# Kernel optimization log

Measured on AMD Instinct MI355X. Metric: run time of the kernel, lower is better.

The kernel has to match this reference:

```python
import jax, jax.numpy as jnp
import numpy as np

HID = 2048
HEADS = 16
HD = HID // HEADS  # 128
EPS = 1e-6


def setup_inputs() -> dict:
    key = jax.random.key(0)
    ks = jax.random.split(key, 9)
    s = 1.0 / np.sqrt(HID)
    return {
        "hidden_states": jax.random.normal(ks[0], (4, 4096, HID), jnp.float32),
        "q_w": jax.random.normal(ks[1], (HID, HID), jnp.float32) * s,
        "q_b": jnp.zeros((HID,), jnp.float32),
        "k_w": jax.random.normal(ks[2], (HID, HID), jnp.float32) * s,
        "k_b": jnp.zeros((HID,), jnp.float32),
        "v_w": jax.random.normal(ks[3], (HID, HID), jnp.float32) * s,
        "v_b": jnp.zeros((HID,), jnp.float32),
        "o_w": jax.random.normal(ks[4], (HID, HID), jnp.float32) * s,
        "o_b": jnp.zeros((HID,), jnp.float32),
    }


def _heads(x, b, s):
    # [B,S,HID] -> [B,H,S,Dh]
    return x.reshape(b, s, HEADS, HD).transpose(0, 2, 1, 3)


def reference(hidden_states, q_w, q_b, k_w, k_b, v_w, v_b, o_w, o_b):
    b, s, _ = hidden_states.shape
    # torch Linear: y = x @ W.T + b
    q = _heads(hidden_states @ q_w.T + q_b, b, s)
    k = _heads(hidden_states @ k_w.T + k_b, b, s)
    v = _heads(hidden_states @ v_w.T + v_b, b, s)
    # kernel feature map: elu(x) + 1
    qp = jax.nn.elu(q) + 1.0
    kp = jax.nn.elu(k) + 1.0
    # KV outer-product reduction over sequence: [B,H,Dh,Dh]
    kv = jnp.einsum('bhsd,bhse->bhde', kp, v)
    # normalizer z = q' @ sum_s k'  -> [B,H,S,1]
    z = jnp.einsum('bhsd,bhd->bhs', qp, kp.sum(axis=2))[..., None]
    attn = jnp.einsum('bhsd,bhde->bhse', qp, kv) / (z + EPS)
    out = attn.transpose(0, 2, 1, 3).reshape(b, s, HID)
    return out @ o_w.T + o_b
```

## Files before the change

### kernel.cpp

```cpp
#include <hip/hip_runtime.h>
#include <hip/hip_bf16.h>

#define HIDC 2048
#define NHEADS 16
#define HDIM 128
#define NB 4
#define NS 4096
#define NROWS (NB*NS)
#define QSTR 6144
#define EPSV 1e-6f

typedef __attribute__((ext_vector_type(8))) short s16x8;
typedef __attribute__((ext_vector_type(4))) float f32x4;
typedef __attribute__((ext_vector_type(8))) unsigned short u16x8;

static __device__ __forceinline__ unsigned short f2b(float f) {
  unsigned int u = __float_as_uint(f);
  u += 0x7fffu + ((u >> 16) & 1u);
  return (unsigned short)(u >> 16);
}
static __device__ __forceinline__ float b2f(unsigned short h) {
  return __uint_as_float(((unsigned int)h) << 16);
}

static __device__ __forceinline__ void gload_lds16(const unsigned short* g, unsigned short* l) {
  __builtin_amdgcn_global_load_lds(
      (const __attribute__((address_space(1))) void*)g,
      (__attribute__((address_space(3))) void*)l, 16, 0, 0);
}

__global__ __launch_bounds__(256) void convert_all(
    const float* __restrict__ hs, const float* __restrict__ qw,
    const float* __restrict__ kw, const float* __restrict__ vw,
    const float* __restrict__ ow,
    unsigned short* __restrict__ hsb, unsigned short* __restrict__ qwb,
    unsigned short* __restrict__ kwb, unsigned short* __restrict__ vwb,
    unsigned short* __restrict__ owb)
{
  int bid = blockIdx.x;
  const float* src; unsigned short* dst; size_t base;
  if (bid < 16384) { src = hs; dst = hsb; base = (size_t)bid << 11; }
  else {
    int t = bid - 16384; int wsel = t >> 11; int wb = t & 2047;
    src = wsel == 0 ? qw : wsel == 1 ? kw : wsel == 2 ? vw : ow;
    dst = wsel == 0 ? qwb : wsel == 1 ? kwb : wsel == 2 ? vwb : owb;
    base = (size_t)wb << 11;
  }
  size_t i = base + ((size_t)threadIdx.x << 3);
  float4 a = *(const float4*)(src + i);
  float4 b = *(const float4*)(src + i + 4);
  u16x8 o;
  o[0] = f2b(a.x); o[1] = f2b(a.y); o[2] = f2b(a.z); o[3] = f2b(a.w);
  o[4] = f2b(b.x); o[5] = f2b(b.y); o[6] = f2b(b.z); o[7] = f2b(b.w);
  *(u16x8*)(dst + i) = o;
}

template<int QKV, int OUT_BF16>
__global__ __launch_bounds__(512, 2) void gemm256(
    const unsigned short* __restrict__ A,
    const unsigned short* __restrict__ B0,
    const unsigned short* __restrict__ B1,
    const unsigned short* __restrict__ B2,
    const float* __restrict__ bias0,
    const float* __restrict__ bias1,
    const float* __restrict__ bias2,
    void* __restrict__ Cp,
    int ntile, int astr, int ostr)
{
  __shared__ unsigned short lds[65536];
  const int tid = threadIdx.x;
  const int lane = tid & 63, wid = tid >> 6;
  const int wr = wid >> 2, wc = wid & 3;
  const int l15 = lane & 15, l4 = lane >> 4;

  const int cpx = (int)gridDim.x >> 3;
  const int bidx = (int)blockIdx.x;
  const int wg = (bidx & 7) * cpx + (bidx >> 3);
  const int csz = ntile << 2;
  const int chunk = wg / csz;
  const int t = wg % csz;
  const int bm = ((chunk << 2) + (t & 3)) << 8;
  const int bn = (t >> 2) << 8;

  const unsigned short* Bp = B0;
  const float* bias = bias0;
  bool act = false;
  int bnw = bn;
  if (QKV) {
    int seg = bn >> 11;
    Bp = seg == 0 ? B0 : (seg == 1 ? B1 : B2);
    bias = seg == 0 ? bias0 : (seg == 1 ? bias1 : bias2);
    act = seg < 2;
    bnw = bn & 2047;
  }

  const int c0 = wid << 1;
  const int srow = lane >> 2;
  const int scol = (((lane & 3) ^ ((srow >> 1) & 3)) << 3);
  const unsigned short* Asrc0 = A + (size_t)(bm + (c0 << 4) + srow) * astr + scol;
  const unsigned short* Asrc1 = Asrc0 + (size_t)16 * astr;
  const unsigned short* Bsrc0 = Bp + (size_t)(bnw + (c0 << 4) + srow) * HIDC + scol;
  const unsigned short* Bsrc1 = Bsrc0 + (size_t)16 * HIDC;
  const int adst = c0 << 9;

  const int xa = ((l4 ^ ((l15 >> 1) & 3)) << 3);
  const int abase = ((wr << 7) + l15) * 32 + xa;
  const int bbase = 8192 + ((wc << 6) + l15) * 32 + xa;

  f32x4 acc[8][4] = {};
  s16x8 bfr[2][4];
  s16x8 alo[2][4];
  s16x8 ahi[4];

#define STAGE_A(s_) { const int sl_ = ((s_) & 3) << 14; const int kt_ = (s_) << 5; \
    gload_lds16(Asrc0 + kt_, &lds[sl_ + adst]); \
    gload_lds16(Asrc1 + kt_, &lds[sl_ + adst + 512]); }
#define STAGE_B(s_) { const int sl_ = ((s_) & 3) << 14; const int kt_ = (s_) << 5; \
    gload_lds16(Bsrc0 + kt_, &lds[sl_ + 8192 + adst]); \
    gload_lds16(Bsrc1 + kt_, &lds[sl_ + 8192 + adst + 512]); }

#define MM4(ai_, r_, P_) { \
    acc[r_][0] = __builtin_amdgcn_mfma_f32_16x16x32_bf16(ai_, bfr[P_][0], acc[r_][0], 0, 0, 0); \
    acc[r_][1] = __builtin_amdgcn_mfma_f32_16x16x32_bf16(ai_, bfr[P_][1], acc[r_][1], 0, 0, 0); \
    acc[r_][2] = __builtin_amdgcn_mfma_f32_16x16x32_bf16(ai_, bfr[P_][2], acc[r_][2], 0, 0, 0); \
    acc[r_][3] = __builtin_amdgcn_mfma_f32_16x16x32_bf16(ai_, bfr[P_][3], acc[r_][3], 0, 0, 0); }

#define DO_STEP(s_, P_, STG, GATE, NEXT) { \
    const int sl = ((s_) & 3) << 14; \
     \
    ahi[0] = *(const s16x8*)&lds[sl + abase + 2048]; \
    ahi[1] = *(const s16x8*)&lds[sl + abase + 2560]; \
    ahi[2] = *(const s16x8*)&lds[sl + abase + 3072]; \
    ahi[3] = *(const s16x8*)&lds[sl + abase + 3584]; \
    if (STG) STAGE_A((s_) + 3); \
    __builtin_amdgcn_sched_barrier(0); \
    __builtin_amdgcn_s_setprio(1); \
    MM4(alo[P_][0], 0, P_) MM4(alo[P_][1], 1, P_) \
    MM4(alo[P_][2], 2, P_) MM4(alo[P_][3], 3, P_) \
    __builtin_amdgcn_s_setprio(0); \
    if ((GATE) == 6)      { asm volatile("s_waitcnt vmcnt(6)" ::: "memory"); } \
    else if ((GATE) == 4) { asm volatile("s_waitcnt vmcnt(4)" ::: "memory"); } \
    else if ((GATE) == 0) { asm volatile("s_waitcnt vmcnt(0)" ::: "memory"); } \
    __builtin_amdgcn_s_barrier(); \
     \
    if (NEXT) { \
      const int sln = (((s_) + 1) & 3) << 14; \
      bfr[1-(P_)][0] = *(const s16x8*)&lds[sln + bbase]; \
      bfr[1-(P_)][1] = *(const s16x8*)&lds[sln + bbase + 512]; \
      bfr[1-(P_)][2] = *(const s16x8*)&lds[sln + bbase + 1024]; \
      bfr[1-(P_)][3] = *(const s16x8*)&lds[sln + bbase + 1536]; \
      alo[1-(P_)][0] = *(const s16x8*)&lds[sln + abase]; \
      alo[1-(P_)][1] = *(const s16x8*)&lds[sln + abase + 512]; \
      alo[1-(P_)][2] = *(const s16x8*)&lds[sln + abase + 1024]; \
      alo[1-(P_)][3] = *(const s16x8*)&lds[sln + abase + 1536]; \
    } \
    if (STG) STAGE_B((s_) + 3); \
    __builtin_amdgcn_sched_barrier(0); \
    __builtin_amdgcn_s_setprio(1); \
    MM4(ahi[0], 4, P_) MM4(ahi[1], 5, P_) \
    MM4(ahi[2], 6, P_) MM4(ahi[3], 7, P_) \
    __builtin_amdgcn_s_setprio(0); \
    __builtin_amdgcn_s_barrier(); \
  }

  STAGE_A(0); STAGE_B(0);
  STAGE_A(1); STAGE_B(1);
  STAGE_A(2); STAGE_B(2);
  asm volatile("s_waitcnt vmcnt(8)" ::: "memory");
  __builtin_amdgcn_s_barrier();
  bfr[0][0] = *(const s16x8*)&lds[bbase];
  bfr[0][1] = *(const s16x8*)&lds[bbase + 512];
  bfr[0][2] = *(const s16x8*)&lds[bbase + 1024];
  bfr[0][3] = *(const s16x8*)&lds[bbase + 1536];
  alo[0][0] = *(const s16x8*)&lds[abase];
  alo[0][1] = *(const s16x8*)&lds[abase + 512];
  alo[0][2] = *(const s16x8*)&lds[abase + 1024];
  alo[0][3] = *(const s16x8*)&lds[abase + 1536];

  for (int s = 0; s < 60; s += 2) {
    DO_STEP(s,     0, 1, 6, 1)
    DO_STEP(s + 1, 1, 1, 6, 1)
  }
  DO_STEP(60, 0, 1, 6, 1)
  DO_STEP(61, 1, 0, 4, 1)
  DO_STEP(62, 0, 0, 0, 1)
  DO_STEP(63, 1, 0, -1, 0)

#undef DO_STEP
#undef MM4
#undef STAGE_A
#undef STAGE_B

  #pragma unroll
  for (int nf = 0; nf < 4; ++nf) {
    const int colw = (wc << 6) + (nf << 4) + l15;
    const float bv = bias[bnw + colw];
    #pragma unroll
    for (int mf = 0; mf < 8; ++mf) {
      #pragma unroll
      for (int r = 0; r < 4; ++r) {
        const int row = bm + (wr << 7) + (mf << 4) + (l4 << 2) + r;
        float v = acc[mf][nf][r] + bv;
        if (QKV) { if (act) v = (v > 0.f) ? (v + 1.f) : __expf(v); }
        const size_t off = (size_t)row * ostr + bn + colw;
        if (OUT_BF16) ((unsigned short*)Cp)[off] = f2b(v);
        else          ((float*)Cp)[off] = v;
      }
    }
  }
}

__global__ __launch_bounds__(256) void kv_partial(
    const unsigned short* __restrict__ kp, const unsigned short* __restrict__ vv,
    float* __restrict__ kvp, float* __restrict__ ksp)
{
  const int bh = blockIdx.x >> 4;
  const int chunk = blockIdx.x & 15;
  const int b = bh >> 4, h = bh & 15;
  const int tid = threadIdx.x;
  const int td = tid >> 4, te = tid & 15;

  __shared__ float kpl[32][128];
  __shared__ float vl[32][132];

  float acc[8][8] = {};
  float ks[8] = {};

  const size_t rowbase = (size_t)b * NS * QSTR + (size_t)h * HDIM;
  const int s0 = chunk * 256;

  for (int st = 0; st < 256; st += 32) {
    __syncthreads();
    #pragma unroll
    for (int i = 0; i < 2; ++i) {
      int idx = tid + (i << 8);
      int row = idx >> 4, q = idx & 15;
      size_t g = rowbase + (size_t)(s0 + st + row) * QSTR + (q << 3);
      u16x8 k8 = *(const u16x8*)(kp + g);
      u16x8 v8 = *(const u16x8*)(vv + g);
      float tk[8], tv[8];
      #pragma unroll
      for (int j = 0; j < 8; ++j) { tk[j] = b2f(k8[j]); tv[j] = b2f(v8[j]); }
      *(float4*)&kpl[row][(q << 3)]     = make_float4(tk[0], tk[1], tk[2], tk[3]);
      *(float4*)&kpl[row][(q << 3) + 4] = make_float4(tk[4], tk[5], tk[6], tk[7]);
      *(float4*)&vl[row][(q << 3)]      = make_float4(tv[0], tv[1], tv[2], tv[3]);
      *(float4*)&vl[row][(q << 3) + 4]  = make_float4(tv[4], tv[5], tv[6], tv[7]);
    }
    __syncthreads();
    #pragma unroll 4
    for (int s = 0; s < 32; ++s) {
      float kd[8], ve[8];
      *(float4*)&kd[0] = *(const float4*)&kpl[s][td << 3];
      *(float4*)&kd[4] = *(const float4*)&kpl[s][(td << 3) + 4];
      *(float4*)&ve[0] = *(const float4*)&vl[s][te << 3];
      *(float4*)&ve[4] = *(const float4*)&vl[s][(te << 3) + 4];
      if (te == 0) {
        #pragma unroll
        for (int i = 0; i < 8; ++i) ks[i] += kd[i];
      }
      #pragma unroll
      for (int i = 0; i < 8; ++i)
        #pragma unroll
        for (int j = 0; j < 8; ++j)
          acc[i][j] += kd[i] * ve[j];
    }
  }

  float* outp = kvp + ((size_t)(chunk * 64 + bh) << 14);
  #pragma unroll
  for (int j = 0; j < 8; ++j) {
    int e = (te << 3) + j;
    float r0[8];
    #pragma unroll
    for (int i = 0; i < 8; ++i) r0[i] = acc[i][j];
    *(float4*)&outp[(size_t)e * HDIM + (td << 3)]     = *(float4*)&r0[0];
    *(float4*)&outp[(size_t)e * HDIM + (td << 3) + 4] = *(float4*)&r0[4];
  }
  if (te == 0) {
    float* kso = ksp + ((size_t)(chunk * 64 + bh) << 7) + (td << 3);
    #pragma unroll
    for (int i = 0; i < 8; ++i) kso[i] = ks[i];
  }
}

__global__ __launch_bounds__(256) void kv_reduce(
    const float* __restrict__ kvp, float* __restrict__ kvT)
{
  int i = blockIdx.x * 256 + threadIdx.x;
  float s = 0.f;
  #pragma unroll
  for (int c = 0; c < 16; ++c) s += kvp[(size_t)c * (64 * 16384) + i];
  kvT[i] = s;
}

__global__ __launch_bounds__(256) void attn_ker(
    const unsigned short* __restrict__ qp, const float* __restrict__ kvT,
    const float* __restrict__ ksp, unsigned short* __restrict__ attn)
{
  const int bh = blockIdx.x >> 5, stile = blockIdx.x & 31;
  const int b = bh >> 4, h = bh & 15;
  const int tid = threadIdx.x;
  const int lane = tid & 63, w = tid >> 6;
  const int l15 = lane & 15, l4 = lane >> 4;

  __shared__ unsigned short Qs[128][136];
  __shared__ unsigned short Ks[128][136];
  __shared__ float ksl[128];
  __shared__ float zs[128];

  const size_t qbase = ((size_t)b * NS + (size_t)stile * 128) * QSTR + (size_t)h * HDIM;

  #pragma unroll
  for (int i = 0; i < 8; ++i) {
    int idx = tid + (i << 8);
    int row = idx >> 4, q = idx & 15;
    u16x8 v8 = *(const u16x8*)(qp + qbase + (size_t)row * QSTR + (q << 3));
    *(u16x8*)&Qs[row][q << 3] = v8;
  }
  const float* kvb = kvT + ((size_t)bh << 14);
  #pragma unroll
  for (int i = 0; i < 16; ++i) {
    int idx = tid + (i << 8);
    int row = idx >> 5, q = idx & 31;
    float4 v4 = *(const float4*)(kvb + (size_t)row * HDIM + (q << 2));
    ushort4 w4; w4.x = f2b(v4.x); w4.y = f2b(v4.y); w4.z = f2b(v4.z); w4.w = f2b(v4.w);
    *(ushort4*)&Ks[row][q << 2] = w4;
  }
  if (tid < 128) {
    float s = 0.f;
    #pragma unroll
    for (int c = 0; c < 16; ++c) s += ksp[((size_t)(c * 64 + bh) << 7) + tid];
    ksl[tid] = s;
  }
  __syncthreads();
  if (tid < 128) {
    float z = 0.f;
    #pragma unroll
    for (int dq = 0; dq < 16; ++dq) {
      u16x8 qv = *(const u16x8*)&Qs[tid][dq << 3];
      #pragma unroll
      for (int j = 0; j < 8; ++j) z += b2f(qv[j]) * ksl[(dq << 3) + j];
    }
    zs[tid] = 1.f / (z + EPSV);
  }
  __syncthreads();

  f32x4 acc[2][8] = {};
  #pragma unroll
  for (int kk = 0; kk < 4; ++kk) {
    s16x8 a[2], bb[8];
    #pragma unroll
    for (int mf = 0; mf < 2; ++mf)
      a[mf] = *(const s16x8*)&Qs[(w << 5) + (mf << 4) + l15][(kk << 5) + (l4 << 3)];
    #pragma unroll
    for (int nf = 0; nf < 8; ++nf)
      bb[nf] = *(const s16x8*)&Ks[(nf << 4) + l15][(kk << 5) + (l4 << 3)];
    #pragma unroll
    for (int mf = 0; mf < 2; ++mf)
      #pragma unroll
      for (int nf = 0; nf < 8; ++nf)
        acc[mf][nf] = __builtin_amdgcn_mfma_f32_16x16x32_bf16(a[mf], bb[nf], acc[mf][nf], 0, 0, 0);
  }

  #pragma unroll
  for (int mf = 0; mf < 2; ++mf) {
    #pragma unroll
    for (int r = 0; r < 4; ++r) {
      const int rl = (w << 5) + (mf << 4) + (l4 << 2) + r;
      const float zi = zs[rl];
      #pragma unroll
      for (int nf = 0; nf < 8; ++nf) {
        const int e = (nf << 4) + l15;
        attn[qbase + (size_t)rl * QSTR + e] = f2b(acc[mf][nf][r] * zi);
      }
    }
  }
}

extern "C" void kernel_launch(void* const* d_in, const int* in_sizes, int n_in,
                              void* d_out, int out_size, void* d_ws, size_t ws_size,
                              hipStream_t stream) {
  const float* hs = (const float*)d_in[0];
  const float* qw = (const float*)d_in[1];
  const float* qb = (const float*)d_in[2];
  const float* kw = (const float*)d_in[3];
  const float* kb = (const float*)d_in[4];
  const float* vw = (const float*)d_in[5];
  const float* vb = (const float*)d_in[6];
  const float* ow = (const float*)d_in[7];
  const float* ob = (const float*)d_in[8];

  char* w = (char*)d_ws;
  unsigned short* hsb = (unsigned short*)(w);
  unsigned short* qwb = (unsigned short*)(w + 67108864);
  unsigned short* kwb = (unsigned short*)(w + 75497472);
  unsigned short* vwb = (unsigned short*)(w + 83886080);
  unsigned short* owb = (unsigned short*)(w + 92274688);
  unsigned short* qkv = (unsigned short*)(w + 100663296);
  float* kvp = (float*)(w);
  float* ksp = (float*)(w + 67108864);
  float* kvT = (float*)(w + 67108864 + 524288);

  convert_all<<<dim3(24576), dim3(256), 0, stream>>>(hs, qw, kw, vw, ow, hsb, qwb, kwb, vwb, owb);
  gemm256<1, 1><<<dim3(24 * 64), dim3(512), 0, stream>>>(
      hsb, qwb, kwb, vwb, qb, kb, vb, qkv, 24, HIDC, QSTR);
  kv_partial<<<dim3(1024), dim3(256), 0, stream>>>(qkv + 2048, qkv + 4096, kvp, ksp);
  kv_reduce<<<dim3(4096), dim3(256), 0, stream>>>(kvp, kvT);
  attn_ker<<<dim3(2048), dim3(256), 0, stream>>>(qkv, kvT, ksp, qkv + 4096);
  gemm256<0, 0><<<dim3(8 * 64), dim3(512), 0, stream>>>(
      qkv + 4096, owb, owb, owb, ob, ob, ob, d_out, 8, QSTR, HIDC);
}
```

Before: 764.0 us.

## Restructure GEMM main loop to one barrier per K-step with double-buffered A fragments

The GEMM inner loop now uses a single wait and barrier per K-step instead of two half-steps. Each step loads all 8 A fragments for the next step into a double-buffered register set and loads the 4 B fragments for the current step right after the barrier. It then issues both A and B global-to-LDS stages and runs all 32 MFMAs in one block. This halves barrier and scheduling overhead, but the current step's B LDS reads now sit directly before the MFMAs with less latency hiding.

```diff
diff --git a/kernel.cpp b/kernel.cpp
--- a/kernel.cpp
+++ b/kernel.cpp
@@ -108,9 +108,8 @@
   const int bbase = 8192 + ((wc << 6) + l15) * 32 + xa;
 
   f32x4 acc[8][4] = {};
-  s16x8 bfr[2][4];
-  s16x8 alo[2][4];
-  s16x8 ahi[4];
+  s16x8 af[2][8];
+  s16x8 bfr[4];
 
 #define STAGE_A(s_) { const int sl_ = ((s_) & 3) << 14; const int kt_ = (s_) << 5; \
     gload_lds16(Asrc0 + kt_, &lds[sl_ + adst]); \
@@ -119,48 +118,41 @@
     gload_lds16(Bsrc0 + kt_, &lds[sl_ + 8192 + adst]); \
     gload_lds16(Bsrc1 + kt_, &lds[sl_ + 8192 + adst + 512]); }
 
-#define MM4(ai_, r_, P_) { \
-    acc[r_][0] = __builtin_amdgcn_mfma_f32_16x16x32_bf16(ai_, bfr[P_][0], acc[r_][0], 0, 0, 0); \
-    acc[r_][1] = __builtin_amdgcn_mfma_f32_16x16x32_bf16(ai_, bfr[P_][1], acc[r_][1], 0, 0, 0); \
-    acc[r_][2] = __builtin_amdgcn_mfma_f32_16x16x32_bf16(ai_, bfr[P_][2], acc[r_][2], 0, 0, 0); \
-    acc[r_][3] = __builtin_amdgcn_mfma_f32_16x16x32_bf16(ai_, bfr[P_][3], acc[r_][3], 0, 0, 0); }
-
-#define DO_STEP(s_, P_, STG, GATE, NEXT) { \
+#define MM8(nf_, P_) { \
+    acc[0][nf_] = __builtin_amdgcn_mfma_f32_16x16x32_bf16(af[P_][0], bfr[nf_], acc[0][nf_], 0, 0, 0); \
+    acc[1][nf_] = __builtin_amdgcn_mfma_f32_16x16x32_bf16(af[P_][1], bfr[nf_], acc[1][nf_], 0, 0, 0); \
+    acc[2][nf_] = __builtin_amdgcn_mfma_f32_16x16x32_bf16(af[P_][2], bfr[nf_], acc[2][nf_], 0, 0, 0); \
+    acc[3][nf_] = __builtin_amdgcn_mfma_f32_16x16x32_bf16(af[P_][3], bfr[nf_], acc[3][nf_], 0, 0, 0); \
+    acc[4][nf_] = __builtin_amdgcn_mfma_f32_16x16x32_bf16(af[P_][4], bfr[nf_], acc[4][nf_], 0, 0, 0); \
+    acc[5][nf_] = __builtin_amdgcn_mfma_f32_16x16x32_bf16(af[P_][5], bfr[nf_], acc[5][nf_], 0, 0, 0); \
+    acc[6][nf_] = __builtin_amdgcn_mfma_f32_16x16x32_bf16(af[P_][6], bfr[nf_], acc[6][nf_], 0, 0, 0); \
+    acc[7][nf_] = __builtin_amdgcn_mfma_f32_16x16x32_bf16(af[P_][7], bfr[nf_], acc[7][nf_], 0, 0, 0); }
+
+#define DO_STEP(s_, P_, GATE, DO_A, DO_STG) { \
     const int sl = ((s_) & 3) << 14; \
-     \
-    ahi[0] = *(const s16x8*)&lds[sl + abase + 2048]; \
-    ahi[1] = *(const s16x8*)&lds[sl + abase + 2560]; \
-    ahi[2] = *(const s16x8*)&lds[sl + abase + 3072]; \
-    ahi[3] = *(const s16x8*)&lds[sl + abase + 3584]; \
-    if (STG) STAGE_A((s_) + 3); \
+    if ((GATE) == 4)      { asm volatile("s_waitcnt vmcnt(4)" ::: "memory"); } \
+    else if ((GATE) == 0) { asm volatile("s_waitcnt vmcnt(0)" ::: "memory"); } \
+    __builtin_amdgcn_s_barrier(); \
+    bfr[0] = *(const s16x8*)&lds[sl + bbase]; \
+    bfr[1] = *(const s16x8*)&lds[sl + bbase + 512]; \
+    bfr[2] = *(const s16x8*)&lds[sl + bbase + 1024]; \
+    bfr[3] = *(const s16x8*)&lds[sl + bbase + 1536]; \
+    if (DO_A) { \
+      const int sln = (((s_) + 1) & 3) << 14; \
+      af[1-(P_)][0] = *(const s16x8*)&lds[sln + abase]; \
+      af[1-(P_)][1] = *(const s16x8*)&lds[sln + abase + 512]; \
+      af[1-(P_)][2] = *(const s16x8*)&lds[sln + abase + 1024]; \
+      af[1-(P_)][3] = *(const s16x8*)&lds[sln + abase + 1536]; \
+      af[1-(P_)][4] = *(const s16x8*)&lds[sln + abase + 2048]; \
+      af[1-(P_)][5] = *(const s16x8*)&lds[sln + abase + 2560]; \
+      af[1-(P_)][6] = *(const s16x8*)&lds[sln + abase + 3072]; \
+      af[1-(P_)][7] = *(const s16x8*)&lds[sln + abase + 3584]; \
+    } \
+    if (DO_STG) { STAGE_A((s_) + 3); STAGE_B((s_) + 3); } \
     __builtin_amdgcn_sched_barrier(0); \
     __builtin_amdgcn_s_setprio(1); \
-    MM4(alo[P_][0], 0, P_) MM4(alo[P_][1], 1, P_) \
-    MM4(alo[P_][2], 2, P_) MM4(alo[P_][3], 3, P_) \
+    MM8(0, P_) MM8(1, P_) MM8(2, P_) MM8(3, P_) \
     __builtin_amdgcn_s_setprio(0); \
-    if ((GATE) == 6)      { asm volatile("s_waitcnt vmcnt(6)" ::: "memory"); } \
-    else if ((GATE) == 4) { asm volatile("s_waitcnt vmcnt(4)" ::: "memory"); } \
-    else if ((GATE) == 0) { asm volatile("s_waitcnt vmcnt(0)" ::: "memory"); } \
-    __builtin_amdgcn_s_barrier(); \
-     \
-    if (NEXT) { \
-      const int sln = (((s_) + 1) & 3) << 14; \
-      bfr[1-(P_)][0] = *(const s16x8*)&lds[sln + bbase]; \
-      bfr[1-(P_)][1] = *(const s16x8*)&lds[sln + bbase + 512]; \
-      bfr[1-(P_)][2] = *(const s16x8*)&lds[sln + bbase + 1024]; \
-      bfr[1-(P_)][3] = *(const s16x8*)&lds[sln + bbase + 1536]; \
-      alo[1-(P_)][0] = *(const s16x8*)&lds[sln + abase]; \
-      alo[1-(P_)][1] = *(const s16x8*)&lds[sln + abase + 512]; \
-      alo[1-(P_)][2] = *(const s16x8*)&lds[sln + abase + 1024]; \
-      alo[1-(P_)][3] = *(const s16x8*)&lds[sln + abase + 1536]; \
-    } \
-    if (STG) STAGE_B((s_) + 3); \
-    __builtin_amdgcn_sched_barrier(0); \
-    __builtin_amdgcn_s_setprio(1); \
-    MM4(ahi[0], 4, P_) MM4(ahi[1], 5, P_) \
-    MM4(ahi[2], 6, P_) MM4(ahi[3], 7, P_) \
-    __builtin_amdgcn_s_setprio(0); \
-    __builtin_amdgcn_s_barrier(); \
   }
 
   STAGE_A(0); STAGE_B(0);
@@ -168,26 +160,26 @@
   STAGE_A(2); STAGE_B(2);
   asm volatile("s_waitcnt vmcnt(8)" ::: "memory");
   __builtin_amdgcn_s_barrier();
-  bfr[0][0] = *(const s16x8*)&lds[bbase];
-  bfr[0][1] = *(const s16x8*)&lds[bbase + 512];
-  bfr[0][2] = *(const s16x8*)&lds[bbase + 1024];
-  bfr[0][3] = *(const s16x8*)&lds[bbase + 1536];
-  alo[0][0] = *(const s16x8*)&lds[abase];
-  alo[0][1] = *(const s16x8*)&lds[abase + 512];
-  alo[0][2] = *(const s16x8*)&lds[abase + 1024];
-  alo[0][3] = *(const s16x8*)&lds[abase + 1536];
+  af[0][0] = *(const s16x8*)&lds[abase];
+  af[0][1] = *(const s16x8*)&lds[abase + 512];
+  af[0][2] = *(const s16x8*)&lds[abase + 1024];
+  af[0][3] = *(const s16x8*)&lds[abase + 1536];
+  af[0][4] = *(const s16x8*)&lds[abase + 2048];
+  af[0][5] = *(const s16x8*)&lds[abase + 2560];
+  af[0][6] = *(const s16x8*)&lds[abase + 3072];
+  af[0][7] = *(const s16x8*)&lds[abase + 3584];
 
   for (int s = 0; s < 60; s += 2) {
-    DO_STEP(s,     0, 1, 6, 1)
-    DO_STEP(s + 1, 1, 1, 6, 1)
-  }
-  DO_STEP(60, 0, 1, 6, 1)
-  DO_STEP(61, 1, 0, 4, 1)
-  DO_STEP(62, 0, 0, 0, 1)
-  DO_STEP(63, 1, 0, -1, 0)
+    DO_STEP(s,     0, 4, 1, 1)
+    DO_STEP(s + 1, 1, 4, 1, 1)
+  }
+  DO_STEP(60, 0, 4, 1, 1)
+  DO_STEP(61, 1, 4, 1, 0)
+  DO_STEP(62, 0, 0, 1, 0)
+  DO_STEP(63, 1, -1, 0, 0)
 
 #undef DO_STEP
-#undef MM4
+#undef MM8
 #undef STAGE_A
 #undef STAGE_B
 
```

Result: no change. 777.5 us (+1.8%).
